# Kernel tuning notes

Measured on AMD Instinct MI355X. Metric: run time of the kernel, lower is better.

The kernel has to match this reference:

```python
import jax, jax.numpy as jnp
import numpy as np

EPS = 1e-12  # F.normalize eps


def _l2norm_spatial(x):
    # F.normalize(x, p=2, dim=(2,3)): divide by max(||x||_2 over HxW, eps)
    n = jnp.sqrt(jnp.sum(x * x, axis=(2, 3), keepdims=True))
    return x / jnp.maximum(n, EPS)


def _cscr_forward(rgb, ir):
    C = rgb.shape[1]
    # channel average pooling (cap) and channel max pooling (cmp)
    rgb_cap = jnp.mean(rgb, axis=1, keepdims=True)
    rgb_cmp = jnp.max(rgb, axis=1, keepdims=True)
    ir_cap = jnp.mean(ir, axis=1, keepdims=True)
    ir_cmp = jnp.max(ir, axis=1, keepdims=True)
    # cp = cat([cap,cmp]) summed across modalities; sa = max(cp[:,0::2], cp[:,1::2])
    sa = jnp.maximum(rgb_cap + ir_cap, rgb_cmp + ir_cmp)  # [B,1,H,W]
    sa_sig = jax.nn.sigmoid(sa)

    # cosine similarity of each channel with the (sigmoid'd) spatial attention map
    sa_n = _l2norm_spatial(sa_sig)
    sim_rgb = jnp.sum(sa_n * _l2norm_spatial(rgb), axis=(2, 3))  # [B,C]
    sim_ir = jnp.sum(sa_n * _l2norm_spatial(ir), axis=(2, 3))    # [B,C]

    # sort channels by similarity ascending and gather
    ord_rgb = jnp.argsort(sim_rgb, axis=1)
    ord_ir = jnp.argsort(sim_ir, axis=1)
    sorted_rgb = jnp.take_along_axis(rgb, ord_rgb[:, :, None, None], axis=1)
    sorted_ir = jnp.take_along_axis(ir, ord_ir[:, :, None, None], axis=1)

    # split point = max over batch of #positive similarities (scalar per stream)
    n_rgb = jnp.max(jnp.sum(sim_rgb > 0, axis=1))
    n_ir = jnp.max(jnp.sum(sim_ir > 0, axis=1))

    # When C_rgb == C_ir, torch's equalize_channel_lengths_positive pads the
    # stream with the SMALLER positive count with one extra channel
    # max(sorted_rgb[:, :1], sorted_ir[:, :1]) (the strided slice [::extra] of
    # the first `extra` channels collapses to channel 0), and the subsequent
    # negative truncation drops that stream's last (most positive) channel.
    # The stream with the larger positive count comes out as its full sorted
    # channels. We express that shape-statically with a shifted gather + where.
    extra_fea = jnp.maximum(sorted_rgb[:, :1], sorted_ir[:, :1])  # [B,1,H,W]
    idx = jnp.arange(C)

    def reassemble(sorted_x, n_self, n_other):
        g = jnp.where(idx <= n_self, idx, idx - 1)          # gather with shift after insertion point
        shifted = jnp.take(sorted_x, g, axis=1)             # [B,C,H,W]
        inserted = jnp.where((idx == n_self)[None, :, None, None], extra_fea, shifted)
        return jnp.where(n_other > n_self, inserted, sorted_x)

    rgb_cs = reassemble(sorted_rgb, n_rgb, n_ir)
    ir_cs = reassemble(sorted_ir, n_ir, n_rgb)

    # final spatial-attention gating
    return rgb_cs * sa_sig, ir_cs * sa_sig


def setup_inputs() -> dict:
    key = jax.random.key(0)
    k1, k2 = jax.random.split(key)
    B, C, H, W = 32, 256, 56, 56
    rgb = jax.random.normal(k1, (B, C, H, W), dtype=jnp.float32)
    ir = jax.random.normal(k2, (B, C, H, W), dtype=jnp.float32)
    return {"rgb": rgb, "ir": ir}


def reference(rgb, ir):
    return _cscr_forward(rgb, ir)
```

## Files before the change

### kernel.cpp

```cpp
#include <hip/hip_runtime.h>
#include <math.h>


#define CDIM   256
#define HWDIM  3136
#define CHW    (CDIM * HWDIM)
#define PAIRS  1568
#define QUADS  784

typedef unsigned short u16;
typedef unsigned int   u32;

__device__ __forceinline__ float bf2f(u32 u) { return __uint_as_float(u << 16); }
__device__ __forceinline__ u16  f2bf(float f) {
    u32 x = __float_as_uint(f);
    return (u16)((x + 0x7FFFu + ((x >> 16) & 1u)) >> 16);
}
__device__ __forceinline__ u32 pack2(u32 u, float s0, float s1) {
    float a0 = __uint_as_float(u << 16);
    float a1 = __uint_as_float(u & 0xFFFF0000u);
    u32 lo = f2bf(a0 * s0), hi = f2bf(a1 * s1);
    return lo | (hi << 16);
}
__device__ __forceinline__ u32 maxpack2(u32 u, u32 w, float s0, float s1) {
    float a0 = __uint_as_float(u << 16), a1 = __uint_as_float(u & 0xFFFF0000u);
    float b0 = __uint_as_float(w << 16), b1 = __uint_as_float(w & 0xFFFF0000u);
    u32 lo = f2bf(fmaxf(a0, b0) * s0), hi = f2bf(fmaxf(a1, b1) * s1);
    return lo | (hi << 16);
}

__global__ __launch_bounds__(256) void k_sa(const void* __restrict__ rgb_,
                                            const void* __restrict__ ir_,
                                            int* __restrict__ flg,
                                            float* __restrict__ sa32,
                                            int* __restrict__ nmx) {
    __shared__ int s_det;
    if (threadIdx.x == 0) s_det = 0;
    __syncthreads();
    {
        const u16* r16 = (const u16*)rgb_;
        int w = 0;
        for (int i = threadIdx.x; i < 8192; i += 256) {
            u16 u = r16[i];
            int e = (u >> 7) & 0xFF;
            float v = bf2f((u32)u);
            if (e == 0xFF || fabsf(v) > 1e3f) w++;
        }
        atomicAdd(&s_det, w);
    }
    __syncthreads();
    int md = (s_det > 256) ? 1 : 0;
    if (blockIdx.x == 0 && blockIdx.y == 0 && threadIdx.x == 0) {
        flg[0] = md;
        nmx[0] = 0; nmx[1] = 0;
    }

    int b  = blockIdx.y;
    int g  = threadIdx.x >> 6;
    int ql = blockIdx.x * 64 + (threadIdx.x & 63);
    bool act = ql < QUADS;

    double s0 = 0.0, s1 = 0.0, s2 = 0.0, s3 = 0.0;
    float m0r = -INFINITY, m1r = -INFINITY, m2r = -INFINITY, m3r = -INFINITY;
    float m0i = -INFINITY, m1i = -INFINITY, m2i = -INFINITY, m3i = -INFINITY;

    if (act) {
        if (md == 1) {
            const float4* R = (const float4*)rgb_;
            const float4* I = (const float4*)ir_;
            size_t bq = (size_t)b * (CHW / 4) + ql;
            #pragma unroll 2
            for (int c = g; c < CDIM; c += 4) {
                float4 r = R[bq + (size_t)c * QUADS];
                float4 i = I[bq + (size_t)c * QUADS];
                s0 += (double)r.x + (double)i.x;
                s1 += (double)r.y + (double)i.y;
                s2 += (double)r.z + (double)i.z;
                s3 += (double)r.w + (double)i.w;
                m0r = fmaxf(m0r, r.x); m1r = fmaxf(m1r, r.y);
                m2r = fmaxf(m2r, r.z); m3r = fmaxf(m3r, r.w);
                m0i = fmaxf(m0i, i.x); m1i = fmaxf(m1i, i.y);
                m2i = fmaxf(m2i, i.z); m3i = fmaxf(m3i, i.w);
            }
        } else {
            const u32* R = (const u32*)rgb_;
            const u32* I = (const u32*)ir_;
            size_t bw = (size_t)b * (CHW / 2) + 2 * (size_t)ql;
            #pragma unroll 2
            for (int c = g; c < CDIM; c += 4) {
                size_t o = bw + (size_t)c * PAIRS;
                u32 wr0 = R[o], wr1 = R[o + 1];
                u32 wi0 = I[o], wi1 = I[o + 1];
                float r0 = bf2f(wr0 & 0xFFFFu), r1 = bf2f(wr0 >> 16);
                float r2 = bf2f(wr1 & 0xFFFFu), r3 = bf2f(wr1 >> 16);
                float i0 = bf2f(wi0 & 0xFFFFu), i1 = bf2f(wi0 >> 16);
                float i2 = bf2f(wi1 & 0xFFFFu), i3 = bf2f(wi1 >> 16);
                s0 += (double)r0 + (double)i0;
                s1 += (double)r1 + (double)i1;
                s2 += (double)r2 + (double)i2;
                s3 += (double)r3 + (double)i3;
                m0r = fmaxf(m0r, r0); m1r = fmaxf(m1r, r1);
                m2r = fmaxf(m2r, r2); m3r = fmaxf(m3r, r3);
                m0i = fmaxf(m0i, i0); m1i = fmaxf(m1i, i1);
                m2i = fmaxf(m2i, i2); m3i = fmaxf(m3i, i3);
            }
        }
    }

    __shared__ double shs[4][256];
    __shared__ float  shr[4][256];
    __shared__ float  shi[4][256];
    int t = threadIdx.x;
    shs[0][t] = s0; shs[1][t] = s1; shs[2][t] = s2; shs[3][t] = s3;
    shr[0][t] = m0r; shr[1][t] = m1r; shr[2][t] = m2r; shr[3][t] = m3r;
    shi[0][t] = m0i; shi[1][t] = m1i; shi[2][t] = m2i; shi[3][t] = m3i;
    __syncthreads();
    if (g == 0 && act) {
        #pragma unroll
        for (int k = 1; k < 4; ++k) {
            int t2 = t + 64 * k;
            s0 += shs[0][t2]; s1 += shs[1][t2];
            s2 += shs[2][t2]; s3 += shs[3][t2];
            m0r = fmaxf(m0r, shr[0][t2]); m1r = fmaxf(m1r, shr[1][t2]);
            m2r = fmaxf(m2r, shr[2][t2]); m3r = fmaxf(m3r, shr[3][t2]);
            m0i = fmaxf(m0i, shi[0][t2]); m1i = fmaxf(m1i, shi[1][t2]);
            m2i = fmaxf(m2i, shi[2][t2]); m3i = fmaxf(m3i, shi[3][t2]);
        }
        double sa0 = fmax(s0 * (1.0 / 256.0), (double)m0r + (double)m0i);
        double sa1 = fmax(s1 * (1.0 / 256.0), (double)m1r + (double)m1i);
        double sa2 = fmax(s2 * (1.0 / 256.0), (double)m2r + (double)m2i);
        double sa3 = fmax(s3 * (1.0 / 256.0), (double)m3r + (double)m3i);
        float4 ov;
        ov.x = (float)(1.0 / (1.0 + exp(-sa0)));
        ov.y = (float)(1.0 / (1.0 + exp(-sa1)));
        ov.z = (float)(1.0 / (1.0 + exp(-sa2)));
        ov.w = (float)(1.0 / (1.0 + exp(-sa3)));
        *(float4*)&sa32[(size_t)b * HWDIM + 4 * (size_t)ql] = ov;
    }
}

__global__ __launch_bounds__(256) void k_sim(const void* __restrict__ rgb_,
                                             const void* __restrict__ ir_,
                                             const int* __restrict__ flg,
                                             const float* __restrict__ sa32,
                                             double* __restrict__ sims) {
    __shared__ float s_sa[HWDIM];
    int p0 = blockIdx.x * 4;
    int b  = (p0 >> 8) & 31;
    {
        const float4* src = (const float4*)(sa32 + (size_t)b * HWDIM);
        float4* dst = (float4*)s_sa;
        for (int i = threadIdx.x; i < QUADS; i += 256) dst[i] = src[i];
    }
    __syncthreads();

    int wid = threadIdx.x >> 6, lane = threadIdx.x & 63;
    int p = p0 + wid;
    int stream = p >> 13;
    int md = flg[0];
    int plane = p & 8191;
    const float4* sv = (const float4*)s_sa;

    double ss = 0.0, dot = 0.0;
    if (md == 1) {
        const float4* x = (const float4*)(stream ? ir_ : rgb_) + (size_t)plane * QUADS;
        #pragma unroll 2
        for (int j = lane; j < QUADS; j += 64) {
            float4 v = x[j];
            float4 s = sv[j];
            ss  = fma((double)v.x, (double)v.x,
                  fma((double)v.y, (double)v.y,
                  fma((double)v.z, (double)v.z,
                  fma((double)v.w, (double)v.w, ss))));
            dot = fma((double)s.x, (double)v.x,
                  fma((double)s.y, (double)v.y,
                  fma((double)s.z, (double)v.z,
                  fma((double)s.w, (double)v.w, dot))));
        }
    } else {
        const u32* x = (const u32*)(stream ? ir_ : rgb_) + (size_t)plane * PAIRS;
        #pragma unroll 2
        for (int j = lane; j < QUADS; j += 64) {
            u32 w0 = x[2 * j], w1 = x[2 * j + 1];
            double v0 = (double)bf2f(w0 & 0xFFFFu), v1 = (double)bf2f(w0 >> 16);
            double v2 = (double)bf2f(w1 & 0xFFFFu), v3 = (double)bf2f(w1 >> 16);
            float4 s = sv[j];
            ss  = fma(v0, v0, fma(v1, v1, fma(v2, v2, fma(v3, v3, ss))));
            dot = fma((double)s.x, v0, fma((double)s.y, v1,
                  fma((double)s.z, v2, fma((double)s.w, v3, dot))));
        }
    }
    #pragma unroll
    for (int off = 32; off >= 1; off >>= 1) {
        ss  += __shfl_xor(ss,  off, 64);
        dot += __shfl_xor(dot, off, 64);
    }
    if (lane == 0) {
        double nrm = sqrt(ss);
        if (nrm < 1e-12) nrm = 1e-12;
        sims[p] = dot / nrm;
    }
}

__global__ __launch_bounds__(256) void k_sort(const double* __restrict__ sims,
                                              int* __restrict__ ord,
                                              int* __restrict__ nmx) {
    __shared__ double s[256];
    __shared__ int csum;
    int sb = blockIdx.x;
    int c  = threadIdx.x;
    double v = sims[sb * 256 + c];
    if (isnan(v)) v = -INFINITY;
    s[c] = v;
    if (c == 0) csum = 0;
    __syncthreads();
    int rank = 0;
    #pragma unroll 8
    for (int j = 0; j < 256; ++j) {
        double u = s[j];
        rank += (u < v) || (u == v && j < c);
    }
    ord[sb * 256 + rank] = c;
    unsigned long long m = __ballot(v > 0.0);
    if ((c & 63) == 0) atomicAdd(&csum, (int)__popcll(m));
    __syncthreads();
    if (c == 0) atomicMax(&nmx[sb >> 5], csum);
}

__global__ __launch_bounds__(256) void k_gather(const void* __restrict__ rgb_,
                                                const void* __restrict__ ir_,
                                                const int* __restrict__ flg,
                                                const float* __restrict__ sa32,
                                                const int* __restrict__ ord,
                                                const int* __restrict__ nmax,
                                                void* __restrict__ out_) {
    int sb = blockIdx.x;
    int stream = sb >> 13;
    int b  = (sb >> 8) & 31;
    int co = sb & 255;
    int md = flg[0];
    int n_self  = nmax[stream];
    int n_other = nmax[1 - stream];
    bool insert  = n_other > n_self;
    bool special = insert && (co == n_self);
    int obase = sb & ~255;

    const float*  sig = sa32 + (size_t)b * HWDIM;
    const float4* sg  = (const float4*)sig;

    if (!special) {
        int ci = co;
        if (insert && co > n_self) ci = co - 1;
        int src = ord[obase + ci] & 255;
        size_t pb = (size_t)(b * 256 + src) * HWDIM;
        if (md == 0) {
            const u16* x = stream ? (const u16*)ir_ : (const u16*)rgb_;
            const uint4* xin = (const uint4*)(x + pb);
            uint4* o = (uint4*)((u16*)out_ + (size_t)sb * HWDIM);
            for (int i = threadIdx.x; i < 392; i += 256) {
                uint4 u = xin[i];
                float4 s0 = sg[2 * i], s1 = sg[2 * i + 1];
                uint4 r;
                r.x = pack2(u.x, s0.x, s0.y);
                r.y = pack2(u.y, s0.z, s0.w);
                r.z = pack2(u.z, s1.x, s1.y);
                r.w = pack2(u.w, s1.z, s1.w);
                o[i] = r;
            }
        } else {
            const float* x = stream ? (const float*)ir_ : (const float*)rgb_;
            const float4* xin = (const float4*)(x + pb);
            float4* o = (float4*)((float*)out_ + (size_t)sb * HWDIM);
            for (int i = threadIdx.x; i < 784; i += 256) {
                float4 v = xin[i], s = sg[i];
                o[i] = make_float4(v.x * s.x, v.y * s.y, v.z * s.z, v.w * s.w);
            }
        }
    } else {
        int src_r = ord[b * 256] & 255;
        int src_i = ord[8192 + b * 256] & 255;
        size_t pr = (size_t)(b * 256 + src_r) * HWDIM;
        size_t pi = (size_t)(b * 256 + src_i) * HWDIM;
        if (md == 0) {
            const uint4* xr = (const uint4*)((const u16*)rgb_ + pr);
            const uint4* xi = (const uint4*)((const u16*)ir_  + pi);
            uint4* o = (uint4*)((u16*)out_ + (size_t)sb * HWDIM);
            for (int i = threadIdx.x; i < 392; i += 256) {
                uint4 u = xr[i], w = xi[i];
                float4 s0 = sg[2 * i], s1 = sg[2 * i + 1];
                uint4 r;
                r.x = maxpack2(u.x, w.x, s0.x, s0.y);
                r.y = maxpack2(u.y, w.y, s0.z, s0.w);
                r.z = maxpack2(u.z, w.z, s1.x, s1.y);
                r.w = maxpack2(u.w, w.w, s1.z, s1.w);
                o[i] = r;
            }
        } else {
            const float4* xr = (const float4*)((const float*)rgb_ + pr);
            const float4* xi = (const float4*)((const float*)ir_  + pi);
            float4* o = (float4*)((float*)out_ + (size_t)sb * HWDIM);
            for (int i = threadIdx.x; i < 784; i += 256) {
                float4 u = xr[i], w = xi[i], s = sg[i];
                o[i] = make_float4(fmaxf(u.x, w.x) * s.x, fmaxf(u.y, w.y) * s.y,
                                   fmaxf(u.z, w.z) * s.z, fmaxf(u.w, w.w) * s.w);
            }
        }
    }
}

extern "C" void kernel_launch(void* const* d_in, const int* in_sizes, int n_in,
                              void* d_out, int out_size, void* d_ws, size_t ws_size,
                              hipStream_t stream) {
    const void* rgb = d_in[0];
    const void* ir  = d_in[1];

    char* ws = (char*)d_ws;
    int*    flg  = (int*)   ws;
    float*  sa32 = (float*) (ws + 1024);
    double* sims = (double*)(ws + 402432);
    int*    ord  = (int*)   (ws + 533504);
    int*    nmx  = (int*)   (ws + 599296);

    k_sa    <<<dim3(13, 32), 256, 0, stream>>>(rgb, ir, flg, sa32, nmx);
    k_sim   <<<4096,         256, 0, stream>>>(rgb, ir, flg, sa32, sims);
    k_sort  <<<64,           256, 0, stream>>>(sims, ord, nmx);
    k_gather<<<16384,        256, 0, stream>>>(rgb, ir, flg, sa32, ord, nmx, d_out);
}
```

Baseline: 430.1 us.

## Rework k_sa into single-wave blocks with shuffle reductions and smaller dtype probe

The spatial-attention kernel now runs 64-thread blocks over a finer 49x32 grid, so 16 quads per block are each reduced across four channel groups with wave shuffles instead of shared memory and barriers. The dtype-detection probe shrinks from 8192 halfwords with a block atomic to 128 halfwords reduced by shuffle, using a scaled threshold. The bf16 path reads one uint2 per quad instead of two u32 loads. The aim is more blocks in flight and less per-block overhead in the first kernel, at the cost of a less robust dtype heuristic.

```diff
diff --git a/kernel.cpp b/kernel.cpp
--- a/kernel.cpp
+++ b/kernel.cpp
@@ -29,103 +29,97 @@
     return lo | (hi << 16);
 }
 
-__global__ __launch_bounds__(256) void k_sa(const void* __restrict__ rgb_,
-                                            const void* __restrict__ ir_,
-                                            int* __restrict__ flg,
-                                            float* __restrict__ sa32,
-                                            int* __restrict__ nmx) {
-    __shared__ int s_det;
-    if (threadIdx.x == 0) s_det = 0;
-    __syncthreads();
+__global__ __launch_bounds__(64) void k_sa(const void* __restrict__ rgb_,
+                                           const void* __restrict__ ir_,
+                                           int* __restrict__ flg,
+                                           float* __restrict__ sa32,
+                                           int* __restrict__ nmx) {
+    int lane = threadIdx.x;
+
+    int w = 0;
     {
-        const u16* r16 = (const u16*)rgb_;
-        int w = 0;
-        for (int i = threadIdx.x; i < 8192; i += 256) {
-            u16 u = r16[i];
-            int e = (u >> 7) & 0xFF;
-            float v = bf2f((u32)u);
+        u32 u = ((const u32*)rgb_)[lane];
+        u32 hs[2] = { u & 0xFFFFu, u >> 16 };
+        #pragma unroll
+        for (int k = 0; k < 2; ++k) {
+            int e = (hs[k] >> 7) & 0xFF;
+            float v = bf2f(hs[k]);
             if (e == 0xFF || fabsf(v) > 1e3f) w++;
         }
-        atomicAdd(&s_det, w);
-    }
-    __syncthreads();
-    int md = (s_det > 256) ? 1 : 0;
-    if (blockIdx.x == 0 && blockIdx.y == 0 && threadIdx.x == 0) {
+    }
+    #pragma unroll
+    for (int off = 32; off >= 1; off >>= 1) w += __shfl_xor(w, off, 64);
+    int md = (w > 8) ? 1 : 0;
+    if (blockIdx.x == 0 && blockIdx.y == 0 && lane == 0) {
         flg[0] = md;
         nmx[0] = 0; nmx[1] = 0;
     }
 
     int b  = blockIdx.y;
-    int g  = threadIdx.x >> 6;
-    int ql = blockIdx.x * 64 + (threadIdx.x & 63);
-    bool act = ql < QUADS;
+    int g  = lane >> 4;
+    int ql = blockIdx.x * 16 + (lane & 15);
 
     double s0 = 0.0, s1 = 0.0, s2 = 0.0, s3 = 0.0;
     float m0r = -INFINITY, m1r = -INFINITY, m2r = -INFINITY, m3r = -INFINITY;
     float m0i = -INFINITY, m1i = -INFINITY, m2i = -INFINITY, m3i = -INFINITY;
 
-    if (act) {
-        if (md == 1) {
-            const float4* R = (const float4*)rgb_;
-            const float4* I = (const float4*)ir_;
-            size_t bq = (size_t)b * (CHW / 4) + ql;
-            #pragma unroll 2
-            for (int c = g; c < CDIM; c += 4) {
-                float4 r = R[bq + (size_t)c * QUADS];
-                float4 i = I[bq + (size_t)c * QUADS];
-                s0 += (double)r.x + (double)i.x;
-                s1 += (double)r.y + (double)i.y;
-                s2 += (double)r.z + (double)i.z;
-                s3 += (double)r.w + (double)i.w;
-                m0r = fmaxf(m0r, r.x); m1r = fmaxf(m1r, r.y);
-                m2r = fmaxf(m2r, r.z); m3r = fmaxf(m3r, r.w);
-                m0i = fmaxf(m0i, i.x); m1i = fmaxf(m1i, i.y);
-                m2i = fmaxf(m2i, i.z); m3i = fmaxf(m3i, i.w);
-            }
-        } else {
-            const u32* R = (const u32*)rgb_;
-            const u32* I = (const u32*)ir_;
-            size_t bw = (size_t)b * (CHW / 2) + 2 * (size_t)ql;
-            #pragma unroll 2
-            for (int c = g; c < CDIM; c += 4) {
-                size_t o = bw + (size_t)c * PAIRS;
-                u32 wr0 = R[o], wr1 = R[o + 1];
-                u32 wi0 = I[o], wi1 = I[o + 1];
-                float r0 = bf2f(wr0 & 0xFFFFu), r1 = bf2f(wr0 >> 16);
-                float r2 = bf2f(wr1 & 0xFFFFu), r3 = bf2f(wr1 >> 16);
-                float i0 = bf2f(wi0 & 0xFFFFu), i1 = bf2f(wi0 >> 16);
-                float i2 = bf2f(wi1 & 0xFFFFu), i3 = bf2f(wi1 >> 16);
-                s0 += (double)r0 + (double)i0;
-                s1 += (double)r1 + (double)i1;
-                s2 += (double)r2 + (double)i2;
-                s3 += (double)r3 + (double)i3;
-                m0r = fmaxf(m0r, r0); m1r = fmaxf(m1r, r1);
-                m2r = fmaxf(m2r, r2); m3r = fmaxf(m3r, r3);
-                m0i = fmaxf(m0i, i0); m1i = fmaxf(m1i, i1);
-                m2i = fmaxf(m2i, i2); m3i = fmaxf(m3i, i3);
-            }
-        }
-    }
-
-    __shared__ double shs[4][256];
-    __shared__ float  shr[4][256];
-    __shared__ float  shi[4][256];
-    int t = threadIdx.x;
-    shs[0][t] = s0; shs[1][t] = s1; shs[2][t] = s2; shs[3][t] = s3;
-    shr[0][t] = m0r; shr[1][t] = m1r; shr[2][t] = m2r; shr[3][t] = m3r;
-    shi[0][t] = m0i; shi[1][t] = m1i; shi[2][t] = m2i; shi[3][t] = m3i;
-    __syncthreads();
-    if (g == 0 && act) {
-        #pragma unroll
-        for (int k = 1; k < 4; ++k) {
-            int t2 = t + 64 * k;
-            s0 += shs[0][t2]; s1 += shs[1][t2];
-            s2 += shs[2][t2]; s3 += shs[3][t2];
-            m0r = fmaxf(m0r, shr[0][t2]); m1r = fmaxf(m1r, shr[1][t2]);
-            m2r = fmaxf(m2r, shr[2][t2]); m3r = fmaxf(m3r, shr[3][t2]);
-            m0i = fmaxf(m0i, shi[0][t2]); m1i = fmaxf(m1i, shi[1][t2]);
-            m2i = fmaxf(m2i, shi[2][t2]); m3i = fmaxf(m3i, shi[3][t2]);
-        }
+    if (md == 1) {
+        const float4* R = (const float4*)rgb_ + (size_t)b * (CHW / 4) + ql;
+        const float4* I = (const float4*)ir_  + (size_t)b * (CHW / 4) + ql;
+        #pragma unroll 4
+        for (int k = 0; k < 64; ++k) {
+            size_t o = (size_t)(4 * k + g) * QUADS;
+            float4 r = R[o];
+            float4 i = I[o];
+            s0 += (double)r.x + (double)i.x;
+            s1 += (double)r.y + (double)i.y;
+            s2 += (double)r.z + (double)i.z;
+            s3 += (double)r.w + (double)i.w;
+            m0r = fmaxf(m0r, r.x); m1r = fmaxf(m1r, r.y);
+            m2r = fmaxf(m2r, r.z); m3r = fmaxf(m3r, r.w);
+            m0i = fmaxf(m0i, i.x); m1i = fmaxf(m1i, i.y);
+            m2i = fmaxf(m2i, i.z); m3i = fmaxf(m3i, i.w);
+        }
+    } else {
+        const uint2* R = (const uint2*)rgb_ + (size_t)b * (CHW / 4) + ql;
+        const uint2* I = (const uint2*)ir_  + (size_t)b * (CHW / 4) + ql;
+        #pragma unroll 4
+        for (int k = 0; k < 64; ++k) {
+            size_t o = (size_t)(4 * k + g) * QUADS;
+            uint2 ur = R[o];
+            uint2 ui = I[o];
+            float r0 = bf2f(ur.x & 0xFFFFu), r1 = bf2f(ur.x >> 16);
+            float r2 = bf2f(ur.y & 0xFFFFu), r3 = bf2f(ur.y >> 16);
+            float i0 = bf2f(ui.x & 0xFFFFu), i1 = bf2f(ui.x >> 16);
+            float i2 = bf2f(ui.y & 0xFFFFu), i3 = bf2f(ui.y >> 16);
+            s0 += (double)r0 + (double)i0;
+            s1 += (double)r1 + (double)i1;
+            s2 += (double)r2 + (double)i2;
+            s3 += (double)r3 + (double)i3;
+            m0r = fmaxf(m0r, r0); m1r = fmaxf(m1r, r1);
+            m2r = fmaxf(m2r, r2); m3r = fmaxf(m3r, r3);
+            m0i = fmaxf(m0i, i0); m1i = fmaxf(m1i, i1);
+            m2i = fmaxf(m2i, i2); m3i = fmaxf(m3i, i3);
+        }
+    }
+
+    #pragma unroll
+    for (int off = 16; off <= 32; off <<= 1) {
+        s0 += __shfl_xor(s0, off, 64);
+        s1 += __shfl_xor(s1, off, 64);
+        s2 += __shfl_xor(s2, off, 64);
+        s3 += __shfl_xor(s3, off, 64);
+        m0r = fmaxf(m0r, __shfl_xor(m0r, off, 64));
+        m1r = fmaxf(m1r, __shfl_xor(m1r, off, 64));
+        m2r = fmaxf(m2r, __shfl_xor(m2r, off, 64));
+        m3r = fmaxf(m3r, __shfl_xor(m3r, off, 64));
+        m0i = fmaxf(m0i, __shfl_xor(m0i, off, 64));
+        m1i = fmaxf(m1i, __shfl_xor(m1i, off, 64));
+        m2i = fmaxf(m2i, __shfl_xor(m2i, off, 64));
+        m3i = fmaxf(m3i, __shfl_xor(m3i, off, 64));
+    }
+
+    if (lane < 16) {
         double sa0 = fmax(s0 * (1.0 / 256.0), (double)m0r + (double)m0i);
         double sa1 = fmax(s1 * (1.0 / 256.0), (double)m1r + (double)m1i);
         double sa2 = fmax(s2 * (1.0 / 256.0), (double)m2r + (double)m2i);
@@ -321,8 +315,8 @@
     int*    ord  = (int*)   (ws + 533504);
     int*    nmx  = (int*)   (ws + 599296);
 
-    k_sa    <<<dim3(13, 32), 256, 0, stream>>>(rgb, ir, flg, sa32, nmx);
-    k_sim   <<<4096,         256, 0, stream>>>(rgb, ir, flg, sa32, sims);
-    k_sort  <<<64,           256, 0, stream>>>(sims, ord, nmx);
-    k_gather<<<16384,        256, 0, stream>>>(rgb, ir, flg, sa32, ord, nmx, d_out);
-}
+    k_sa    <<<dim3(49, 32), 64, 0, stream>>>(rgb, ir, flg, sa32, nmx);
+    k_sim   <<<4096,        256, 0, stream>>>(rgb, ir, flg, sa32, sims);
+    k_sort  <<<64,          256, 0, stream>>>(sims, ord, nmx);
+    k_gather<<<16384,       256, 0, stream>>>(rgb, ir, flg, sa32, ord, nmx, d_out);
+}
```

Measured after the change: 427.9 us. No clear change (-0.5%).
